# Performance work log

Hardware: AMD Instinct MI355X
Metric: run time of the kernel (lower is better)

## Reference

```python
import jax, jax.numpy as jnp
import numpy as np
import math

H = 16          # num_heads
BS = 512        # block_size


def setup_inputs() -> dict:
    key = jax.random.key(0)
    ks = jax.random.split(key, 5)
    B, S, D = 2, 8192, 1024
    return {
        "x": jax.random.normal(ks[0], (B, S, D), dtype=jnp.float32),
        "W_qkv": jax.random.normal(ks[1], (D, 3 * D), dtype=jnp.float32) * (1.0 / math.sqrt(D)),
        "b_qkv": jax.random.normal(ks[2], (3 * D,), dtype=jnp.float32) * 0.02,
        "W_out": jax.random.normal(ks[3], (D, D), dtype=jnp.float32) * (1.0 / math.sqrt(D)),
        "b_out": jax.random.normal(ks[4], (D,), dtype=jnp.float32) * 0.02,
    }


def reference(x, W_qkv, b_qkv, W_out, b_out):
    B, S, D = x.shape
    hd = D // H
    nb = S // BS  # S chosen divisible by block_size, so no padding branch
    scale = 1.0 / math.sqrt(hd)

    qkv = (x @ W_qkv + b_qkv).reshape(B, S, 3, H, hd)
    qkv = jnp.transpose(qkv, (2, 0, 3, 1, 4))  # [3, B, H, S, hd]
    q, k, v = qkv[0], qkv[1], qkv[2]

    # split into blocks: [B, H, nb, BS, hd]
    qb = q.reshape(B, H, nb, BS, hd)
    kb = k.reshape(B, H, nb, BS, hd)
    vb = v.reshape(B, H, nb, BS, hd)

    # local block attention (separate softmax, as in original)
    s1 = jnp.einsum('bhnid,bhnjd->bhnij', qb, kb) * scale
    o1 = jnp.einsum('bhnij,bhnjd->bhnid', jax.nn.softmax(s1, axis=-1), vb)

    # next-block (ring) attention with its own softmax, then summed
    kn = jnp.roll(kb, -1, axis=2)
    vn = jnp.roll(vb, -1, axis=2)
    s2 = jnp.einsum('bhnid,bhnjd->bhnij', qb, kn) * scale
    o2 = jnp.einsum('bhnij,bhnjd->bhnid', jax.nn.softmax(s2, axis=-1), vn)

    out = (o1 + o2).reshape(B, H, S, hd)            # [B, H, S, hd]
    out = jnp.transpose(out, (0, 2, 1, 3)).reshape(B, S, D)
    return out @ W_out + b_out
```

## Files before the change

### kernel.cpp

```cpp
#include <hip/hip_runtime.h>
#include <hip/hip_bf16.h>

typedef __attribute__((ext_vector_type(4))) float f32x4;
typedef __attribute__((ext_vector_type(8))) short s16x8;
typedef __attribute__((address_space(3))) unsigned int lds_uint;
typedef __attribute__((address_space(1))) const unsigned int g_uint;

static __device__ __forceinline__ unsigned short f2b(float f) {
    union { __hip_bfloat16 h; unsigned short u; } c;
    c.h = __float2bfloat16(f);
    return c.u;
}

static __device__ __forceinline__ void async_copy16(const void* gsrc, void* ldst) {
    __builtin_amdgcn_global_load_lds((g_uint*)gsrc, (lds_uint*)ldst, 16, 0, 0);
}

__global__ __launch_bounds__(256) void cvt_x_kernel(const float* __restrict__ x,
                                                    unsigned short* __restrict__ xb) {
    long i = ((long)blockIdx.x * 256 + threadIdx.x) * 8;
    float4 a = *(const float4*)(x + i);
    float4 b = *(const float4*)(x + i + 4);
    union { unsigned short s[8]; s16x8 v; } o;
    o.s[0] = f2b(a.x); o.s[1] = f2b(a.y); o.s[2] = f2b(a.z); o.s[3] = f2b(a.w);
    o.s[4] = f2b(b.x); o.s[5] = f2b(b.y); o.s[6] = f2b(b.z); o.s[7] = f2b(b.w);
    *(s16x8*)(xb + i) = o.v;
}

__global__ __launch_bounds__(256) void cvt_wT_kernel(const float* __restrict__ W,
                                                     unsigned short* __restrict__ Wt,
                                                     int K, int N) {
    __shared__ float T[64][65];
    int nbk = K >> 6;
    int bk = blockIdx.x % nbk;
    int bn = blockIdx.x / nbk;
    int t = threadIdx.x;
    int r = t >> 4, c4 = (t & 15) << 2;
#pragma unroll
    for (int rd = 0; rd < 4; ++rd) {
        int row = rd * 16 + r;
        float4 v = *(const float4*)(W + (long)(bk * 64 + row) * N + bn * 64 + c4);
        T[row][c4 + 0] = v.x; T[row][c4 + 1] = v.y;
        T[row][c4 + 2] = v.z; T[row][c4 + 3] = v.w;
    }
    __syncthreads();
#pragma unroll
    for (int rd = 0; rd < 4; ++rd) {
        int nrow = rd * 16 + r;
        union { unsigned short s[4]; unsigned long long u; } o;
#pragma unroll
        for (int j = 0; j < 4; ++j) o.s[j] = f2b(T[c4 + j][nrow]);
        *(unsigned long long*)(Wt + (long)(bn * 64 + nrow) * K + bk * 64 + c4) = o.u;
    }
}

template<int OM>
__global__ __launch_bounds__(512) void gemm256_kernel(const unsigned short* __restrict__ A,
                                                      const unsigned short* __restrict__ Bt,
                                                      const float* __restrict__ bias,
                                                      unsigned short* __restrict__ qkb,
                                                      unsigned short* __restrict__ vT,
                                                      float* __restrict__ Cf,
                                                      int ntileN) {
    __shared__ char lds[131072];
    const int tid = threadIdx.x;
    const int w = tid >> 6, wm = w >> 2, wn = w & 3;
    const int l = tid & 63, c = l & 15, g = l >> 4;
    const int cpx = gridDim.x >> 3;
    const int wg = (blockIdx.x & 7) * cpx + (blockIdx.x >> 3);
    const int tm = wg / ntileN, tn = wg % ntileN;
    const long m0 = (long)tm << 8, n0 = (long)tn << 8;
    const int swg = (g ^ ((c >> 1) & 3)) << 4;
    const int ssch = (tid & 3) ^ ((tid >> 3) & 3);
    const int rb = tid >> 2;

    f32x4 acc[8][4];
#pragma unroll
    for (int i = 0; i < 8; ++i)
#pragma unroll
        for (int j = 0; j < 4; ++j) acc[i][j] = (f32x4){0.f, 0.f, 0.f, 0.f};

#define STG(panel, p0, u, kh, isB) do { \
    char* blk_ = lds + ((isB) ? 65536 : 0) + (((((u) & 1) * 2 + (kh))) << 14); \
    const unsigned short* sp_ = (panel) + (u) * 64 + (kh) * 32 + ssch * 8; \
    async_copy16(sp_ + ((p0) + rb) * 1024L, blk_ + tid * 16); \
    async_copy16(sp_ + ((p0) + 128 + rb) * 1024L, blk_ + 8192 + tid * 16); \
} while (0)

    STG(Bt, n0, 0, 0, 1); STG(A, m0, 0, 0, 0); STG(Bt, n0, 0, 1, 1); STG(A, m0, 0, 1, 0);
    STG(Bt, n0, 1, 0, 1); STG(A, m0, 1, 0, 0); STG(Bt, n0, 1, 1, 1);
    asm volatile("s_waitcnt vmcnt(10)");
    __builtin_amdgcn_s_barrier();
    __builtin_amdgcn_sched_barrier(0);

#define PHASE_MFMA(IBASE) \
    __builtin_amdgcn_s_setprio(1); \
    _Pragma("unroll") for (int i_ = 0; i_ < 4; ++i_) \
    _Pragma("unroll") for (int j_ = 0; j_ < 4; ++j_) \
        acc[(IBASE) + i_][j_] = __builtin_amdgcn_mfma_f32_16x16x32_bf16(af[i_], bf[j_], acc[(IBASE) + i_][j_], 0, 0, 0); \
    __builtin_amdgcn_s_setprio(0);

#define GSTEP(s, ST1, ST2, ST3, ST4, VMID, VEND) do { \
    const int buf_ = (s) & 1; \
    const char* LA0 = lds + ((buf_ * 2 + 0) << 14); \
    const char* LA1 = lds + ((buf_ * 2 + 1) << 14); \
    const char* LB0 = lds + 65536 + ((buf_ * 2 + 0) << 14); \
    const char* LB1 = lds + 65536 + ((buf_ * 2 + 1) << 14); \
    s16x8 af[4], bf[4]; \
     \
    _Pragma("unroll") for (int i = 0; i < 4; ++i) af[i] = *(const s16x8*)(LA0 + (wm * 128 + i * 16 + c) * 64 + swg); \
    _Pragma("unroll") for (int j = 0; j < 4; ++j) bf[j] = *(const s16x8*)(LB0 + (wn * 64 + j * 16 + c) * 64 + swg); \
    if (ST1) STG(A, m0, (s) + 1, 1, 0); \
    __builtin_amdgcn_s_barrier(); \
    PHASE_MFMA(0) \
    __builtin_amdgcn_s_barrier(); \
    __builtin_amdgcn_sched_barrier(0); \
     \
    _Pragma("unroll") for (int i = 0; i < 4; ++i) af[i] = *(const s16x8*)(LA0 + (wm * 128 + (4 + i) * 16 + c) * 64 + swg); \
    if (ST2) STG(Bt, n0, (s) + 2, 0, 1); \
    __builtin_amdgcn_s_barrier(); \
    PHASE_MFMA(4) \
    asm volatile("s_waitcnt " VMID); \
    __builtin_amdgcn_s_barrier(); \
    __builtin_amdgcn_sched_barrier(0); \
     \
    _Pragma("unroll") for (int i = 0; i < 4; ++i) af[i] = *(const s16x8*)(LA1 + (wm * 128 + i * 16 + c) * 64 + swg); \
    _Pragma("unroll") for (int j = 0; j < 4; ++j) bf[j] = *(const s16x8*)(LB1 + (wn * 64 + j * 16 + c) * 64 + swg); \
    if (ST3) STG(A, m0, (s) + 2, 0, 0); \
    __builtin_amdgcn_s_barrier(); \
    PHASE_MFMA(0) \
    __builtin_amdgcn_s_barrier(); \
    __builtin_amdgcn_sched_barrier(0); \
     \
    _Pragma("unroll") for (int i = 0; i < 4; ++i) af[i] = *(const s16x8*)(LA1 + (wm * 128 + (4 + i) * 16 + c) * 64 + swg); \
    if (ST4) STG(Bt, n0, (s) + 2, 1, 1); \
    __builtin_amdgcn_s_barrier(); \
    PHASE_MFMA(4) \
    if (VEND) { asm volatile("s_waitcnt " VMID##_E); } \
    __builtin_amdgcn_s_barrier(); \
    __builtin_amdgcn_sched_barrier(0); \
} while (0)

#define VM10 "vmcnt(10)"
#define VM10_E "vmcnt(10)"
#define VM8 "vmcnt(8)"
#define VM8_E "vmcnt(4)"
#define VM0 "vmcnt(0)"
#define VM0_E "vmcnt(0)"

    for (int s = 0; s < 14; ++s) GSTEP(s, 1, 1, 1, 1, VM10, 1);
    GSTEP(14, 1, 0, 0, 0, VM8, 1);
    GSTEP(15, 0, 0, 0, 0, VM0, 0);

    const long mrow0 = m0 + wm * 128;
    const int ncol0 = (int)n0 + wn * 64;
    if (OM == 0) {
        if (ncol0 < 2048) {
#pragma unroll
            for (int j = 0; j < 4; ++j) {
                int n = ncol0 + j * 16 + c;
                float bv = bias[n];
#pragma unroll
                for (int i = 0; i < 8; ++i)
#pragma unroll
                    for (int r = 0; r < 4; ++r) {
                        long m = mrow0 + i * 16 + 4 * g + r;
                        qkb[m * 2048 + n] = f2b(acc[i][j][r] + bv);
                    }
            }
        } else {
#pragma unroll
            for (int j = 0; j < 4; ++j) {
                int n = ncol0 + j * 16 + c;
                float bv = bias[n];
                int h = (n - 2048) >> 6, hd = n & 63;
#pragma unroll
                for (int i = 0; i < 8; ++i) {
                    long m = mrow0 + i * 16 + 4 * g;
                    long bb = m >> 13, ss = m & 8191;
                    union { unsigned short sh[4]; unsigned long long u; } o;
#pragma unroll
                    for (int r = 0; r < 4; ++r) o.sh[r] = f2b(acc[i][j][r] + bv);
                    *(unsigned long long*)(vT + ((bb * 16 + h) * 64 + hd) * 8192 + ss) = o.u;
                }
            }
        }
    } else {
#pragma unroll
        for (int j = 0; j < 4; ++j) {
            int n = ncol0 + j * 16 + c;
            float bv = bias[n];
#pragma unroll
            for (int i = 0; i < 8; ++i)
#pragma unroll
                for (int r = 0; r < 4; ++r) {
                    long m = mrow0 + i * 16 + 4 * g + r;
                    Cf[m * 1024 + n] = acc[i][j][r] + bv;
                }
        }
    }
#undef STG
#undef PHASE_MFMA
#undef GSTEP
}

__global__ __launch_bounds__(256) void attn_kernel(const unsigned short* __restrict__ qkb,
                                                   const unsigned short* __restrict__ vT,
                                                   unsigned short* __restrict__ outp) {
    __shared__ unsigned short Ks[64 * 72];
    __shared__ unsigned short VTs[64 * 72];
    __shared__ unsigned short Pws[4][32 * 72];
    const int bid = blockIdx.x;
    const int wgid = (bid & 7) * 256 + (bid >> 3);
    const int qt = wgid & 3;
    const int nblk = (wgid >> 2) & 15;
    const int h = (wgid >> 6) & 15;
    const int b = wgid >> 10;
    const int tid = threadIdx.x;
    const int w = tid >> 6, l = tid & 63;
    const int c = l & 15, g = l >> 4;

    const long qrow0 = (long)b * 8192 + nblk * 512 + qt * 128 + w * 32 + c;
    s16x8 qf[2][2];
#pragma unroll
    for (int qg = 0; qg < 2; ++qg) {
        const unsigned short* qp = qkb + (qrow0 + qg * 16) * 2048 + h * 64;
        qf[qg][0] = *(const s16x8*)(qp + g * 8);
        qf[qg][1] = *(const s16x8*)(qp + 32 + g * 8);
    }

    char* pw = (char*)(&Pws[w][0]);
    const float C2 = 0.125f * 1.44269504088896f;

    const int cc = tid & 7;
    const int rbase = tid >> 3;
    char* kwp = (char*)Ks + rbase * 144 + cc * 16;
    char* vwp = (char*)VTs + rbase * 144 + cc * 16;

    const int kb1 = (nblk + 1) & 15;
    const unsigned short* Kg0 = qkb + ((long)b * 8192 + nblk * 512) * 2048 + 1024 + h * 64
                                + (long)rbase * 2048 + cc * 8;
    const unsigned short* Kg1 = qkb + ((long)b * 8192 + kb1 * 512) * 2048 + 1024 + h * 64
                                + (long)rbase * 2048 + cc * 8;
    const unsigned short* Vg0 = vT + ((long)(b * 16 + h) * 64 + rbase) * 8192 + nblk * 512 + cc * 8;
    const unsigned short* Vg1 = vT + ((long)(b * 16 + h) * 64 + rbase) * 8192 + kb1 * 512 + cc * 8;

    float outv[2][16];
#pragma unroll
    for (int qg = 0; qg < 2; ++qg)
#pragma unroll
        for (int i = 0; i < 16; ++i) outv[qg][i] = 0.f;

    f32x4 oac[2][4];
#pragma unroll
    for (int qg = 0; qg < 2; ++qg)
#pragma unroll
        for (int i = 0; i < 4; ++i) oac[qg][i] = (f32x4){0.f, 0.f, 0.f, 0.f};
    float mrun[2] = {-3e38f, -3e38f}, lrun[2] = {0.f, 0.f};

    s16x8 kreg0 = *(const s16x8*)(Kg0);
    s16x8 kreg1 = *(const s16x8*)(Kg0 + 32 * 2048);
    s16x8 vreg0 = *(const s16x8*)(Vg0);
    s16x8 vreg1 = *(const s16x8*)(Vg0 + 32 * 8192);

    for (int it = 0; it < 16; ++it) {
        __syncthreads();
        *(s16x8*)(kwp) = kreg0;
        *(s16x8*)(kwp + 32 * 144) = kreg1;
        *(s16x8*)(vwp) = vreg0;
        *(s16x8*)(vwp + 32 * 144) = vreg1;
        {
            int itn = it + 1;
            const unsigned short* kn = ((itn & 8) ? Kg1 : Kg0) + ((itn & 7) << 17);
            const unsigned short* vn = ((itn & 8) ? Vg1 : Vg0) + ((itn & 7) << 6);
            kreg0 = *(const s16x8*)(kn);
            kreg1 = *(const s16x8*)(kn + 32 * 2048);
            vreg0 = *(const s16x8*)(vn);
            vreg1 = *(const s16x8*)(vn + 32 * 8192);
        }
        __syncthreads();

        f32x4 sac[2][4];
#pragma unroll
        for (int qg = 0; qg < 2; ++qg)
#pragma unroll
            for (int i = 0; i < 4; ++i) sac[qg][i] = (f32x4){0.f, 0.f, 0.f, 0.f};
#pragma unroll
        for (int kt = 0; kt < 4; ++kt) {
            const char* kr = (const char*)Ks + (kt * 16 + c) * 144 + g * 16;
            s16x8 a0 = *(const s16x8*)(kr);
            s16x8 a1 = *(const s16x8*)(kr + 64);
            sac[0][kt] = __builtin_amdgcn_mfma_f32_16x16x32_bf16(a0, qf[0][0], sac[0][kt], 0, 0, 0);
            sac[0][kt] = __builtin_amdgcn_mfma_f32_16x16x32_bf16(a1, qf[0][1], sac[0][kt], 0, 0, 0);
            sac[1][kt] = __builtin_amdgcn_mfma_f32_16x16x32_bf16(a0, qf[1][0], sac[1][kt], 0, 0, 0);
            sac[1][kt] = __builtin_amdgcn_mfma_f32_16x16x32_bf16(a1, qf[1][1], sac[1][kt], 0, 0, 0);
        }

#pragma unroll
        for (int qg = 0; qg < 2; ++qg) {
            float mx = sac[qg][0][0];
#pragma unroll
            for (int kt = 0; kt < 4; ++kt)
#pragma unroll
                for (int r = 0; r < 4; ++r) mx = fmaxf(mx, sac[qg][kt][r]);
            mx = fmaxf(mx, __shfl_xor(mx, 16, 64));
            mx = fmaxf(mx, __shfl_xor(mx, 32, 64));
            float mnew = fmaxf(mrun[qg], mx);
            float alpha = exp2f((mrun[qg] - mnew) * C2);
            float ls = 0.f;
#pragma unroll
            for (int kt = 0; kt < 4; ++kt) {
                union { unsigned short sh[4]; unsigned long long u; } pk;
#pragma unroll
                for (int r = 0; r < 4; ++r) {
                    float e = exp2f((sac[qg][kt][r] - mnew) * C2);
                    ls += e;
                    pk.sh[r] = f2b(e);
                }
                *(unsigned long long*)(pw + (qg * 16 + c) * 144 + kt * 32 + g * 8) = pk.u;
            }
            ls += __shfl_xor(ls, 16, 64);
            ls += __shfl_xor(ls, 32, 64);
            lrun[qg] = lrun[qg] * alpha + ls;
            mrun[qg] = mnew;
#pragma unroll
            for (int i = 0; i < 4; ++i) oac[qg][i] *= alpha;
        }

#pragma unroll
        for (int kf = 0; kf < 2; ++kf) {
            s16x8 pf0 = *(const s16x8*)(pw + c * 144 + kf * 64 + g * 16);
            s16x8 pf1 = *(const s16x8*)(pw + (16 + c) * 144 + kf * 64 + g * 16);
#pragma unroll
            for (int ht = 0; ht < 4; ++ht) {
                s16x8 vf = *(const s16x8*)((const char*)VTs + (ht * 16 + c) * 144 + kf * 64 + g * 16);
                oac[0][ht] = __builtin_amdgcn_mfma_f32_16x16x32_bf16(vf, pf0, oac[0][ht], 0, 0, 0);
                oac[1][ht] = __builtin_amdgcn_mfma_f32_16x16x32_bf16(vf, pf1, oac[1][ht], 0, 0, 0);
            }
        }

        if ((it & 7) == 7) {
#pragma unroll
            for (int qg = 0; qg < 2; ++qg) {
                float inv = 1.f / lrun[qg];
#pragma unroll
                for (int i = 0; i < 16; ++i) outv[qg][i] += oac[qg][i >> 2][i & 3] * inv;
#pragma unroll
                for (int i = 0; i < 4; ++i) oac[qg][i] = (f32x4){0.f, 0.f, 0.f, 0.f};
                mrun[qg] = -3e38f;
                lrun[qg] = 0.f;
            }
        }
    }

#pragma unroll
    for (int qg = 0; qg < 2; ++qg) {
        unsigned short* op = outp + (qrow0 + qg * 16) * 1024 + h * 64;
#pragma unroll
        for (int ht = 0; ht < 4; ++ht) {
            union { unsigned short sh[4]; unsigned long long u; } o;
#pragma unroll
            for (int r = 0; r < 4; ++r) o.sh[r] = f2b(outv[qg][ht * 4 + r]);
            *(unsigned long long*)(op + ht * 16 + 4 * g) = o.u;
        }
    }
}

extern "C" void kernel_launch(void* const* d_in, const int* in_sizes, int n_in,
                              void* d_out, int out_size, void* d_ws, size_t ws_size,
                              hipStream_t stream) {
    const float* x    = (const float*)d_in[0];
    const float* Wqkv = (const float*)d_in[1];
    const float* bqkv = (const float*)d_in[2];
    const float* Wout = (const float*)d_in[3];
    const float* bout = (const float*)d_in[4];
    float* out = (float*)d_out;

    char* ws = (char*)d_ws;
    unsigned short* xbf   = (unsigned short*)ws;
    unsigned short* wqkvT = (unsigned short*)(ws + 33554432);
    unsigned short* woutT = (unsigned short*)(ws + 39845888);
    unsigned short* qkb   = (unsigned short*)(ws + 41943040);
    unsigned short* vT    = (unsigned short*)(ws + 109051904);
    unsigned short* attn  = xbf;

    cvt_x_kernel<<<8192, 256, 0, stream>>>(x, xbf);
    cvt_wT_kernel<<<(1024 / 64) * (3072 / 64), 256, 0, stream>>>(Wqkv, wqkvT, 1024, 3072);
    cvt_wT_kernel<<<(1024 / 64) * (1024 / 64), 256, 0, stream>>>(Wout, woutT, 1024, 1024);
    gemm256_kernel<0><<<64 * 12, 512, 0, stream>>>(xbf, wqkvT, bqkv, qkb, vT, nullptr, 12);
    attn_kernel<<<2048, 256, 0, stream>>>(qkb, vT, attn);
    gemm256_kernel<1><<<64 * 4, 512, 0, stream>>>(attn, woutT, bout, nullptr, nullptr, out, 4);
}
```

Before: 452.2 us.

## Double-buffer attention K/V tiles via async global-to-LDS copies with XOR swizzle

```diff
diff --git a/kernel.cpp b/kernel.cpp
--- a/kernel.cpp
+++ b/kernel.cpp
@@ -107,7 +107,6 @@
     const char* LB0 = lds + 65536 + ((buf_ * 2 + 0) << 14); \
     const char* LB1 = lds + 65536 + ((buf_ * 2 + 1) << 14); \
     s16x8 af[4], bf[4]; \
-     \
     _Pragma("unroll") for (int i = 0; i < 4; ++i) af[i] = *(const s16x8*)(LA0 + (wm * 128 + i * 16 + c) * 64 + swg); \
     _Pragma("unroll") for (int j = 0; j < 4; ++j) bf[j] = *(const s16x8*)(LB0 + (wn * 64 + j * 16 + c) * 64 + swg); \
     if (ST1) STG(A, m0, (s) + 1, 1, 0); \
@@ -115,7 +114,6 @@
     PHASE_MFMA(0) \
     __builtin_amdgcn_s_barrier(); \
     __builtin_amdgcn_sched_barrier(0); \
-     \
     _Pragma("unroll") for (int i = 0; i < 4; ++i) af[i] = *(const s16x8*)(LA0 + (wm * 128 + (4 + i) * 16 + c) * 64 + swg); \
     if (ST2) STG(Bt, n0, (s) + 2, 0, 1); \
     __builtin_amdgcn_s_barrier(); \
@@ -123,7 +121,6 @@
     asm volatile("s_waitcnt " VMID); \
     __builtin_amdgcn_s_barrier(); \
     __builtin_amdgcn_sched_barrier(0); \
-     \
     _Pragma("unroll") for (int i = 0; i < 4; ++i) af[i] = *(const s16x8*)(LA1 + (wm * 128 + i * 16 + c) * 64 + swg); \
     _Pragma("unroll") for (int j = 0; j < 4; ++j) bf[j] = *(const s16x8*)(LB1 + (wn * 64 + j * 16 + c) * 64 + swg); \
     if (ST3) STG(A, m0, (s) + 2, 0, 0); \
@@ -131,7 +128,6 @@
     PHASE_MFMA(0) \
     __builtin_amdgcn_s_barrier(); \
     __builtin_amdgcn_sched_barrier(0); \
-     \
     _Pragma("unroll") for (int i = 0; i < 4; ++i) af[i] = *(const s16x8*)(LA1 + (wm * 128 + (4 + i) * 16 + c) * 64 + swg); \
     if (ST4) STG(Bt, n0, (s) + 2, 1, 1); \
     __builtin_amdgcn_s_barrier(); \
@@ -207,8 +203,7 @@
 __global__ __launch_bounds__(256) void attn_kernel(const unsigned short* __restrict__ qkb,
                                                    const unsigned short* __restrict__ vT,
                                                    unsigned short* __restrict__ outp) {
-    __shared__ unsigned short Ks[64 * 72];
-    __shared__ unsigned short VTs[64 * 72];
+    __shared__ __align__(16) char KV[4][8192];
     __shared__ unsigned short Pws[4][32 * 72];
     const int bid = blockIdx.x;
     const int wgid = (bid & 7) * 256 + (bid >> 3);
@@ -232,25 +227,30 @@
     char* pw = (char*)(&Pws[w][0]);
     const float C2 = 0.125f * 1.44269504088896f;
 
-    const int cc = tid & 7;
-    const int rbase = tid >> 3;
-    char* kwp = (char*)Ks + rbase * 144 + cc * 16;
-    char* vwp = (char*)VTs + rbase * 144 + cc * 16;
-
+    const int cl = tid & 7, rw = tid >> 3;
+    const int sc = cl ^ (rw & 7);
     const int kb1 = (nblk + 1) & 15;
-    const unsigned short* Kg0 = qkb + ((long)b * 8192 + nblk * 512) * 2048 + 1024 + h * 64
-                                + (long)rbase * 2048 + cc * 8;
-    const unsigned short* Kg1 = qkb + ((long)b * 8192 + kb1 * 512) * 2048 + 1024 + h * 64
-                                + (long)rbase * 2048 + cc * 8;
-    const unsigned short* Vg0 = vT + ((long)(b * 16 + h) * 64 + rbase) * 8192 + nblk * 512 + cc * 8;
-    const unsigned short* Vg1 = vT + ((long)(b * 16 + h) * 64 + rbase) * 8192 + kb1 * 512 + cc * 8;
+    const unsigned short* Kg0 = qkb + ((long)b * 8192 + nblk * 512 + rw) * 2048 + 1024 + h * 64 + sc * 8;
+    const unsigned short* Kg1 = qkb + ((long)b * 8192 + kb1 * 512 + rw) * 2048 + 1024 + h * 64 + sc * 8;
+    const unsigned short* Vg0 = vT + ((long)(b * 16 + h) * 64 + rw) * 8192 + nblk * 512 + sc * 8;
+    const unsigned short* Vg1 = vT + ((long)(b * 16 + h) * 64 + rw) * 8192 + kb1 * 512 + sc * 8;
+
+#define STAGE(tile) do { \
+    const unsigned short* kn_ = (((tile) & 8) ? Kg1 : Kg0) + ((long)((tile) & 7) << 17); \
+    const unsigned short* vn_ = (((tile) & 8) ? Vg1 : Vg0) + (((tile) & 7) << 6); \
+    char* kd_ = KV[(tile) & 1] + tid * 16; \
+    char* vd_ = KV[2 + ((tile) & 1)] + tid * 16; \
+    async_copy16(kn_, kd_); \
+    async_copy16(kn_ + 32L * 2048, kd_ + 4096); \
+    async_copy16(vn_, vd_); \
+    async_copy16(vn_ + 32L * 8192, vd_ + 4096); \
+} while (0)
 
     float outv[2][16];
 #pragma unroll
     for (int qg = 0; qg < 2; ++qg)
 #pragma unroll
         for (int i = 0; i < 16; ++i) outv[qg][i] = 0.f;
-
     f32x4 oac[2][4];
 #pragma unroll
     for (int qg = 0; qg < 2; ++qg)
@@ -258,43 +258,40 @@
         for (int i = 0; i < 4; ++i) oac[qg][i] = (f32x4){0.f, 0.f, 0.f, 0.f};
     float mrun[2] = {-3e38f, -3e38f}, lrun[2] = {0.f, 0.f};
 
-    s16x8 kreg0 = *(const s16x8*)(Kg0);
-    s16x8 kreg1 = *(const s16x8*)(Kg0 + 32 * 2048);
-    s16x8 vreg0 = *(const s16x8*)(Vg0);
-    s16x8 vreg1 = *(const s16x8*)(Vg0 + 32 * 8192);
+    const int ch0 = (g ^ (c & 7)) << 4;
+
+    STAGE(0);
 
     for (int it = 0; it < 16; ++it) {
-        __syncthreads();
-        *(s16x8*)(kwp) = kreg0;
-        *(s16x8*)(kwp + 32 * 144) = kreg1;
-        *(s16x8*)(vwp) = vreg0;
-        *(s16x8*)(vwp + 32 * 144) = vreg1;
-        {
-            int itn = it + 1;
-            const unsigned short* kn = ((itn & 8) ? Kg1 : Kg0) + ((itn & 7) << 17);
-            const unsigned short* vn = ((itn & 8) ? Vg1 : Vg0) + ((itn & 7) << 6);
-            kreg0 = *(const s16x8*)(kn);
-            kreg1 = *(const s16x8*)(kn + 32 * 2048);
-            vreg0 = *(const s16x8*)(vn);
-            vreg1 = *(const s16x8*)(vn + 32 * 8192);
-        }
-        __syncthreads();
+        if (it < 15) {
+            STAGE(it + 1);
+            asm volatile("s_waitcnt vmcnt(4)" ::: "memory");
+        } else {
+            asm volatile("s_waitcnt vmcnt(0)" ::: "memory");
+        }
+        __builtin_amdgcn_s_barrier();
+        __builtin_amdgcn_sched_barrier(0);
+
+        const char* Kc = KV[it & 1];
+        const char* Vc = KV[2 + (it & 1)];
 
         f32x4 sac[2][4];
 #pragma unroll
         for (int qg = 0; qg < 2; ++qg)
 #pragma unroll
             for (int i = 0; i < 4; ++i) sac[qg][i] = (f32x4){0.f, 0.f, 0.f, 0.f};
+        __builtin_amdgcn_s_setprio(1);
 #pragma unroll
         for (int kt = 0; kt < 4; ++kt) {
-            const char* kr = (const char*)Ks + (kt * 16 + c) * 144 + g * 16;
-            s16x8 a0 = *(const s16x8*)(kr);
-            s16x8 a1 = *(const s16x8*)(kr + 64);
+            const char* kr = Kc + (kt * 16 + c) * 128;
+            s16x8 a0 = *(const s16x8*)(kr + ch0);
+            s16x8 a1 = *(const s16x8*)(kr + (ch0 ^ 64));
             sac[0][kt] = __builtin_amdgcn_mfma_f32_16x16x32_bf16(a0, qf[0][0], sac[0][kt], 0, 0, 0);
             sac[0][kt] = __builtin_amdgcn_mfma_f32_16x16x32_bf16(a1, qf[0][1], sac[0][kt], 0, 0, 0);
             sac[1][kt] = __builtin_amdgcn_mfma_f32_16x16x32_bf16(a0, qf[1][0], sac[1][kt], 0, 0, 0);
             sac[1][kt] = __builtin_amdgcn_mfma_f32_16x16x32_bf16(a1, qf[1][1], sac[1][kt], 0, 0, 0);
         }
+        __builtin_amdgcn_s_setprio(0);
 
 #pragma unroll
         for (int qg = 0; qg < 2; ++qg) {
@@ -319,30 +316,33 @@
                 }
                 *(unsigned long long*)(pw + (qg * 16 + c) * 144 + kt * 32 + g * 8) = pk.u;
             }
-            ls += __shfl_xor(ls, 16, 64);
-            ls += __shfl_xor(ls, 32, 64);
             lrun[qg] = lrun[qg] * alpha + ls;
             mrun[qg] = mnew;
 #pragma unroll
             for (int i = 0; i < 4; ++i) oac[qg][i] *= alpha;
         }
 
+        __builtin_amdgcn_s_setprio(1);
 #pragma unroll
         for (int kf = 0; kf < 2; ++kf) {
             s16x8 pf0 = *(const s16x8*)(pw + c * 144 + kf * 64 + g * 16);
             s16x8 pf1 = *(const s16x8*)(pw + (16 + c) * 144 + kf * 64 + g * 16);
 #pragma unroll
             for (int ht = 0; ht < 4; ++ht) {
-                s16x8 vf = *(const s16x8*)((const char*)VTs + (ht * 16 + c) * 144 + kf * 64 + g * 16);
+                s16x8 vf = *(const s16x8*)(Vc + (ht * 16 + c) * 128 + (ch0 ^ (kf << 6)));
                 oac[0][ht] = __builtin_amdgcn_mfma_f32_16x16x32_bf16(vf, pf0, oac[0][ht], 0, 0, 0);
                 oac[1][ht] = __builtin_amdgcn_mfma_f32_16x16x32_bf16(vf, pf1, oac[1][ht], 0, 0, 0);
             }
         }
+        __builtin_amdgcn_s_setprio(0);
 
         if ((it & 7) == 7) {
 #pragma unroll
             for (int qg = 0; qg < 2; ++qg) {
-                float inv = 1.f / lrun[qg];
+                float lt = lrun[qg];
+                lt += __shfl_xor(lt, 16, 64);
+                lt += __shfl_xor(lt, 32, 64);
+                float inv = 1.f / lt;
 #pragma unroll
                 for (int i = 0; i < 16; ++i) outv[qg][i] += oac[qg][i >> 2][i & 3] * inv;
 #pragma unroll
@@ -351,7 +351,11 @@
                 lrun[qg] = 0.f;
             }
         }
-    }
+        __builtin_amdgcn_sched_barrier(0);
+        __builtin_amdgcn_s_barrier();
+        __builtin_amdgcn_sched_barrier(0);
+    }
+#undef STAGE
 
 #pragma unroll
     for (int qg = 0; qg < 2; ++qg) {
```

Measured after the change: 431.9 us. -4.5%, faster.
